# Optimization experiments

Measured on AMD Instinct MI355X. Metric: run time of the kernel, lower is better.

Reference implementation:

```python
import jax, jax.numpy as jnp
import numpy as np

N = 8192          # total genes
B = 16            # number of ragged batch groups (equal-size here: 512 each)
D = 768           # hidden_dim
NEG = -1.0e9      # mask fill value used by the original module


def setup_inputs() -> dict:
    key = jax.random.key(0)
    ks = jax.random.split(key, 10)
    s = 0.02
    inp = {
        "gene_embeddings": jax.random.normal(ks[0], (N, D), dtype=jnp.float32),
        # sorted group ids: 16 contiguous groups of 512 genes
        "batch": (jnp.arange(N) // (N // B)).astype(jnp.int64),
        "Wq": jax.random.normal(ks[1], (D, D), dtype=jnp.float32) * s,
        "bq": jnp.zeros((D,), dtype=jnp.float32),
        "Wk": jax.random.normal(ks[2], (D, D), dtype=jnp.float32) * s,
        "bk": jnp.zeros((D,), dtype=jnp.float32),
        "Wv": jax.random.normal(ks[3], (D, D), dtype=jnp.float32) * s,
        "bv": jnp.zeros((D,), dtype=jnp.float32),
        "Wo": jax.random.normal(ks[4], (D, D), dtype=jnp.float32) * s,
        "bo": jnp.zeros((D,), dtype=jnp.float32),
        "beta": jnp.ones((1,), dtype=jnp.float32) * 0.1,
    }
    return inp


def reference(gene_embeddings, batch, Wq, bq, Wk, bk, Wv, bv, Wo, bo, beta):
    # Single-head attention over full hidden_dim (num_heads unused in original).
    x = gene_embeddings
    q = x @ Wq.T + bq                      # [N, D]
    k = x @ Wk.T + bk
    v = x @ Wv.T + bv
    scale = 1.0 / jnp.sqrt(jnp.asarray(D, dtype=x.dtype))
    scores = (q @ k.T) * scale             # [N, N]
    # block-diagonal group mask + diagonal self-mask (same -1e9 fill as torch code)
    same_group = batch[:, None] == batch[None, :]
    eye = jnp.eye(N, dtype=bool)
    allow = same_group & (~eye)
    scores = jnp.where(allow, scores, NEG)
    weights = jax.nn.softmax(scores, axis=-1)   # dropout in eval mode -> identity
    dyn = weights @ v                       # [N, D]
    dyn = dyn @ Wo.T + bo
    return x + beta * dyn
```

## Files before the change

### kernel.cpp

```cpp
#include <hip/hip_runtime.h>
#include <hip/hip_bf16.h>
#include <cstdint>

using u16 = unsigned short;
using u32 = unsigned int;

typedef __bf16 bf16x8 __attribute__((ext_vector_type(8)));
typedef float  f32x4  __attribute__((ext_vector_type(4)));

__device__ __forceinline__ u32 f2b2(float a, float b) {
    __hip_bfloat162 h = __float22bfloat162_rn(float2{a, b});
    u32 u;
    __builtin_memcpy(&u, &h, 4);
    return u;
}
__device__ __forceinline__ float b2f(u16 b) {
    u32 u = (u32)b << 16;
    float f;
    __builtin_memcpy(&f, &u, 4);
    return f;
}

__device__ __forceinline__ void gload_lds16(const u16* g, u16* l) {
    __builtin_amdgcn_global_load_lds(
        (const __attribute__((address_space(1))) void*)g,
        (__attribute__((address_space(3))) void*)l,
        16, 0, 0);
}

__launch_bounds__(256)
__global__ void pack_kernel(const float* __restrict__ x,
                            const float* __restrict__ Wq,
                            const float* __restrict__ Wk,
                            const float* __restrict__ Wv,
                            const float* __restrict__ Wo,
                            const float* __restrict__ bq,
                            const float* __restrict__ bk,
                            const float* __restrict__ bv,
                            const float* __restrict__ bo,
                            u16* __restrict__ xb,
                            u16* __restrict__ Wqkvb,
                            u16* __restrict__ Wob,
                            u16* __restrict__ WvTb,
                            float* __restrict__ bqk,
                            float* __restrict__ bvoo)
{
    __shared__ u16 tl[64][72];
    const int b = blockIdx.x, tid = threadIdx.x;

    if (b < 3936) {
        int c = b * 256 + tid;
        long e = (long)c * 8;
        const float* src; u16* dst; long off;
        if (e < 6291456L)      { src = x;  dst = xb;             off = e; }
        else if (e < 6881280L) { src = Wq; dst = Wqkvb;          off = e - 6291456L; }
        else if (e < 7471104L) { src = Wk; dst = Wqkvb + 589824; off = e - 6881280L; }
        else                   { src = Wo; dst = Wob;            off = e - 7471104L; }
        float4 v0 = *(const float4*)(src + off);
        float4 v1 = *(const float4*)(src + off + 4);
        uint4 o;
        o.x = f2b2(v0.x, v0.y); o.y = f2b2(v0.z, v0.w);
        o.z = f2b2(v1.x, v1.y); o.w = f2b2(v1.z, v1.w);
        *(uint4*)(dst + off) = o;
        if (c < 768)       bqk[c] = bq[c];
        else if (c < 1536) bqk[c] = bk[c - 768];
    } else if (b < 4080) {
        int t = b - 3936;
        int tr = t / 12, tc = t % 12;
        int lr = tid >> 2, lcb = (tid & 3) * 16;
        const float* src = Wv + (long)(tr * 64 + lr) * 768 + tc * 64 + lcb;
#pragma unroll
        for (int q = 0; q < 4; q++) {
            float4 v = *(const float4*)(src + q * 4);
            u32 p0 = f2b2(v.x, v.y), p1 = f2b2(v.z, v.w);
            tl[lr][lcb + q * 4 + 0] = (u16)p0;
            tl[lr][lcb + q * 4 + 1] = (u16)(p0 >> 16);
            tl[lr][lcb + q * 4 + 2] = (u16)p1;
            tl[lr][lcb + q * 4 + 3] = (u16)(p1 >> 16);
        }
        __syncthreads();
        int li = tid >> 2, lkb = (tid & 3) * 16;
        u16 o[16];
#pragma unroll
        for (int j = 0; j < 16; j++) o[j] = tl[lkb + j][li];
        u16* dst = WvTb + (long)(tc * 64 + li) * 768 + tr * 64 + lkb;
#pragma unroll
        for (int j = 0; j < 16; j++) dst[j] = o[j];
    } else {
        int wave = tid >> 6, lane = tid & 63;
        int j = (b - 4080) * 4 + wave;
        float acc = 0.f;
#pragma unroll
        for (int i = 0; i < 12; i++) {
            int k = i * 64 + lane;
            acc += Wo[(long)j * 768 + k] * bv[k];
        }
#pragma unroll
        for (int d = 32; d; d >>= 1) acc += __shfl_xor(acc, d);
        if (lane == 0) bvoo[j] = acc + bo[j];
    }
}

template<int TM, int TN, int MODE>
__device__ __forceinline__ void gemm_body(
        const u16* __restrict__ A, int lda, long sAz,
        const u16* __restrict__ B, int ldb, long sBz,
        void* __restrict__ Cv, int ldc, long sCz,
        int K,
        const float* __restrict__ bias,
        float scale,
        u16* __restrict__ vTout)
{
    constexpr int FI = TM / 32;
    constexpr int FJ = TN / 32;
    constexpr int CA = TM / 64;
    constexpr int CB = TN / 64;

    __shared__ u16 As[2][TM * 32];
    __shared__ u16 Bs[2][TN * 32];

    const int tid  = threadIdx.x;
    const int g    = blockIdx.z;
    const u16* Ab = A + (long)g * sAz + (long)blockIdx.y * TM * lda;
    const u16* Bb = B + (long)g * sBz + (long)blockIdx.x * TN * ldb;

    const int wave = tid >> 6, lane = tid & 63;
    const int wm = (wave >> 1) * (TM / 2), wn = (wave & 1) * (TN / 2);
    const int ln15 = lane & 15, lq = lane >> 4;

    f32x4 acc[FI][FJ];
#pragma unroll
    for (int i = 0; i < FI; i++)
#pragma unroll
        for (int j = 0; j < FJ; j++)
            acc[i][j] = (f32x4){0.f, 0.f, 0.f, 0.f};

    const int srow = lane >> 2;
    const int sc   = ((lane & 3) ^ ((lane >> 4) & 3)) * 8;
    const u16* Ag[CA]; const u16* Bg[CB];
    int Al[CA], Bl[CB];
#pragma unroll
    for (int t = 0; t < CA; t++) {
        int c = wave * CA + t;
        Ag[t] = Ab + (long)(c * 16 + srow) * lda + sc;
        Al[t] = c * 512;
    }
#pragma unroll
    for (int t = 0; t < CB; t++) {
        int c = wave * CB + t;
        Bg[t] = Bb + (long)(c * 16 + srow) * ldb + sc;
        Bl[t] = c * 512;
    }

    const int foff = ln15 * 32 + ((lq ^ (ln15 >> 2)) * 8);
    const int nk = K >> 5;

#pragma unroll
    for (int t = 0; t < CA; t++) gload_lds16(Ag[t], &As[0][Al[t]]);
#pragma unroll
    for (int t = 0; t < CB; t++) gload_lds16(Bg[t], &Bs[0][Bl[t]]);

    for (int kt = 0; kt < nk; kt++) {
        const int cur = kt & 1;
        __syncthreads();
        if (kt + 1 < nk) {
            const int k0 = (kt + 1) * 32, nxt = cur ^ 1;
#pragma unroll
            for (int t = 0; t < CA; t++) gload_lds16(Ag[t] + k0, &As[nxt][Al[t]]);
#pragma unroll
            for (int t = 0; t < CB; t++) gload_lds16(Bg[t] + k0, &Bs[nxt][Bl[t]]);
        }

        bf16x8 af[FI], bfr[FJ];
#pragma unroll
        for (int i = 0; i < FI; i++)
            af[i] = *(const bf16x8*)&As[cur][(wm / 16 + i) * 512 + foff];
#pragma unroll
        for (int j = 0; j < FJ; j++)
            bfr[j] = *(const bf16x8*)&Bs[cur][(wn / 16 + j) * 512 + foff];
#pragma unroll
        for (int i = 0; i < FI; i++)
#pragma unroll
            for (int j = 0; j < FJ; j++)
                acc[i][j] = __builtin_amdgcn_mfma_f32_16x16x32_bf16(af[i], bfr[j], acc[i][j], 0, 0, 0);
    }

    const int baseRow = blockIdx.y * TM + wm;
    const int baseCol = blockIdx.x * TN + wn;

    if constexpr (MODE == 0) {
        if (baseCol < 1536) {
            u16* C = (u16*)Cv;
#pragma unroll
            for (int i = 0; i < FI; i++)
#pragma unroll
                for (int j = 0; j < FJ; j++) {
                    int col = baseCol + j * 16 + ln15;
                    float bb = bias[col];
                    u32 p01 = f2b2(acc[i][j][0] + bb, acc[i][j][1] + bb);
                    u32 p23 = f2b2(acc[i][j][2] + bb, acc[i][j][3] + bb);
                    long r0 = (long)(baseRow + i * 16 + lq * 4) * ldc + col;
                    C[r0]           = (u16)p01;
                    C[r0 + ldc]     = (u16)(p01 >> 16);
                    C[r0 + 2 * ldc] = (u16)p23;
                    C[r0 + 3 * ldc] = (u16)(p23 >> 16);
                }
        } else {
#pragma unroll
            for (int i = 0; i < FI; i++)
#pragma unroll
                for (int j = 0; j < FJ; j++) {
                    int col = baseCol + j * 16 + ln15;
                    uint2 o;
                    o.x = f2b2(acc[i][j][0], acc[i][j][1]);
                    o.y = f2b2(acc[i][j][2], acc[i][j][3]);
                    *(uint2*)(vTout + (long)(col - 1536) * 8192
                              + baseRow + i * 16 + lq * 4) = o;
                }
        }
    } else if constexpr (MODE == 5) {
        u16* C = (u16*)Cv + (long)g * sCz;
#pragma unroll
        for (int i = 0; i < FI; i++)
#pragma unroll
            for (int j = 0; j < FJ; j++) {
                int col = baseCol + j * 16 + ln15;
                float v[4];
#pragma unroll
                for (int r = 0; r < 4; r++) {
                    int row = baseRow + i * 16 + lq * 4 + r;
                    v[r] = acc[i][j][r] * scale;
                    if (row == col) v[r] = -1.0e9f;
                }
                u32 p01 = f2b2(v[0], v[1]);
                u32 p23 = f2b2(v[2], v[3]);
                long r0 = (long)(baseRow + i * 16 + lq * 4) * ldc + col;
                C[r0]           = (u16)p01;
                C[r0 + ldc]     = (u16)(p01 >> 16);
                C[r0 + 2 * ldc] = (u16)p23;
                C[r0 + 3 * ldc] = (u16)(p23 >> 16);
            }
    } else {
        u16* C = (u16*)Cv;
#pragma unroll
        for (int i = 0; i < FI; i++)
#pragma unroll
            for (int j = 0; j < FJ; j++) {
                int col = baseCol + j * 16 + ln15;
                u32 p01 = f2b2(acc[i][j][0], acc[i][j][1]);
                u32 p23 = f2b2(acc[i][j][2], acc[i][j][3]);
                long r0 = (long)(baseRow + i * 16 + lq * 4) * ldc + col;
                C[r0]           = (u16)p01;
                C[r0 + ldc]     = (u16)(p01 >> 16);
                C[r0 + 2 * ldc] = (u16)p23;
                C[r0 + 3 * ldc] = (u16)(p23 >> 16);
            }
    }
}

__launch_bounds__(256)
__global__ void k_wvo(const u16* A, const u16* B, void* C)
{
    gemm_body<64, 128, 3>(A, 768, 0, B, 768, 0, C, 768, 0, 768,
                          nullptr, 0.f, nullptr);
}
__launch_bounds__(256)
__global__ void k_qkv(const u16* A, const u16* B, void* C, const float* bias,
                      u16* vTout)
{
    gemm_body<128, 128, 0>(A, 768, 0, B, 768, 0, C, 1536, 0, 768,
                           bias, 0.f, vTout);
}
__launch_bounds__(256)
__global__ void k_scores(const u16* A, const u16* B, void* C, float scale)
{
    gemm_body<64, 128, 5>(A, 1536, 512L * 1536, B, 1536, 512L * 1536,
                          C, 512, 512L * 512, 768,
                          nullptr, scale, nullptr);
}

__launch_bounds__(256)
__global__ void k_pvwfused(const u16* __restrict__ S,
                           const u16* __restrict__ vwT,
                           const u16* __restrict__ xb,
                           float* __restrict__ out,
                           const float* __restrict__ bvoo,
                           const float* __restrict__ betaPtr)
{
    __shared__ u16 Pl[32 * 512];
    __shared__ u16 Vs[2][128 * 32];

    const int ct = blockIdx.x, rt = blockIdx.y, g = blockIdx.z;
    const int tid = threadIdx.x;
    const int wave = tid >> 6, lane = tid & 63;
    const int ln15 = lane & 15, lq = lane >> 4;

    const int srow = lane >> 2;
    const int sc   = ((lane & 3) ^ ((lane >> 4) & 3)) * 8;
    const u16* Bg[2]; int Bl[2];
#pragma unroll
    for (int t = 0; t < 2; t++) {
        int c = wave * 2 + t;
        Bg[t] = vwT + (long)(ct * 128 + c * 16 + srow) * 8192 + g * 512 + sc;
        Bl[t] = c * 512;
    }
    gload_lds16(Bg[0], &Vs[0][Bl[0]]);
    gload_lds16(Bg[1], &Vs[0][Bl[1]]);

    const int r   = tid >> 3;
    const int seg = tid & 7;
    const u16* Srow = S + (long)g * 262144 + (long)(rt * 32 + r) * 512 + seg * 64;
    float e[64];
    float m = -3.0e38f;
#pragma unroll
    for (int j = 0; j < 8; j++) {
        uint4 q = *(const uint4*)(Srow + j * 8);
        u32 w[4] = {q.x, q.y, q.z, q.w};
#pragma unroll
        for (int h = 0; h < 4; h++) {
            float lo = b2f((u16)w[h]);
            float hi = b2f((u16)(w[h] >> 16));
            e[j * 8 + h * 2]     = lo;
            e[j * 8 + h * 2 + 1] = hi;
            m = fmaxf(m, fmaxf(lo, hi));
        }
    }
    m = fmaxf(m, __shfl_xor(m, 1));
    m = fmaxf(m, __shfl_xor(m, 2));
    m = fmaxf(m, __shfl_xor(m, 4));
    float sum = 0.f;
#pragma unroll
    for (int j = 0; j < 64; j++) { e[j] = __expf(e[j] - m); sum += e[j]; }
    sum += __shfl_xor(sum, 1);
    sum += __shfl_xor(sum, 2);
    sum += __shfl_xor(sum, 4);
    const float inv = 1.0f / sum;
#pragma unroll
    for (int jj = 0; jj < 8; jj++) {
        uint4 o;
        o.x = f2b2(e[jj * 8 + 0] * inv, e[jj * 8 + 1] * inv);
        o.y = f2b2(e[jj * 8 + 2] * inv, e[jj * 8 + 3] * inv);
        o.z = f2b2(e[jj * 8 + 4] * inv, e[jj * 8 + 5] * inv);
        o.w = f2b2(e[jj * 8 + 6] * inv, e[jj * 8 + 7] * inv);
        int c = seg * 8 + jj;
        *(uint4*)&Pl[(r * 64 + (c ^ (r & 7))) * 8] = o;
    }

    const int wm = (wave >> 1) * 16;
    const int wn = (wave & 1) * 64;
    const int foff = ln15 * 32 + ((lq ^ (ln15 >> 2)) * 8);
    const int prow = wm + ln15;

    f32x4 acc[4];
#pragma unroll
    for (int j = 0; j < 4; j++) acc[j] = (f32x4){0.f, 0.f, 0.f, 0.f};

    for (int kt = 0; kt < 16; kt++) {
        const int cur = kt & 1;
        __syncthreads();
        if (kt + 1 < 16) {
            const int k0 = (kt + 1) * 32, nxt = cur ^ 1;
            gload_lds16(Bg[0] + k0, &Vs[nxt][Bl[0]]);
            gload_lds16(Bg[1] + k0, &Vs[nxt][Bl[1]]);
        }
        bf16x8 ap = *(const bf16x8*)&Pl[(prow * 64 + ((kt * 4 + lq) ^ (prow & 7))) * 8];
        bf16x8 bfr[4];
#pragma unroll
        for (int j = 0; j < 4; j++)
            bfr[j] = *(const bf16x8*)&Vs[cur][(wn / 16 + j) * 512 + foff];
#pragma unroll
        for (int j = 0; j < 4; j++)
            acc[j] = __builtin_amdgcn_mfma_f32_16x16x32_bf16(ap, bfr[j], acc[j], 0, 0, 0);
    }

    const float bet = betaPtr[0];
    const long rowBase = (long)(g * 512 + rt * 32 + wm + lq * 4);
    const u16* Xr = xb + rowBase * 768;
    float* O = out + rowBase * 768;
#pragma unroll
    for (int j = 0; j < 4; j++) {
        int col = ct * 128 + wn + j * 16 + ln15;
        float bb = bvoo[col];
#pragma unroll
        for (int rr = 0; rr < 4; rr++)
            O[rr * 768 + col] = b2f(Xr[rr * 768 + col])
                                + bet * (acc[j][rr] + bb);
    }
}

extern "C" void kernel_launch(void* const* d_in, const int* in_sizes, int n_in,
                              void* d_out, int out_size, void* d_ws, size_t ws_size,
                              hipStream_t stream)
{
    const float* x    = (const float*)d_in[0];
    const float* Wq   = (const float*)d_in[2];
    const float* bq   = (const float*)d_in[3];
    const float* Wk   = (const float*)d_in[4];
    const float* bk   = (const float*)d_in[5];
    const float* Wv   = (const float*)d_in[6];
    const float* bv   = (const float*)d_in[7];
    const float* Wo   = (const float*)d_in[8];
    const float* bo   = (const float*)d_in[9];
    const float* beta = (const float*)d_in[10];
    float* out = (float*)d_out;

    char* ws = (char*)d_ws;
    u16*   qk    = (u16*)(ws + 0);
    u16*   vwT   = (u16*)(ws + 25165824);
    u16*   xb    = (u16*)(ws + 37748736);
    u16*   S     = (u16*)(ws + 50331648);
    u16*   Wqkvb = (u16*)(ws + 58720256);
    u16*   Wob   = (u16*)(ws + 62259200);
    u16*   WvTb  = (u16*)(ws + 63438848);
    float* bqk   = (float*)(ws + 64618496);
    float* bvoo  = (float*)(ws + 64624640);

    const float scale = 0.03608439182435161f;

    pack_kernel<<<4272, 256, 0, stream>>>(x, Wq, Wk, Wv, Wo, bq, bk, bv, bo,
                                          xb, Wqkvb, Wob, WvTb, bqk, bvoo);

    k_wvo<<<dim3(6, 12, 1), 256, 0, stream>>>(Wob, WvTb,
                                              (void*)(Wqkvb + 1536L * 768));

    k_qkv<<<dim3(18, 64, 1), 256, 0, stream>>>(xb, Wqkvb, (void*)qk, bqk, vwT);

    k_scores<<<dim3(4, 8, 16), 256, 0, stream>>>(qk, qk + 768, (void*)S, scale);

    k_pvwfused<<<dim3(6, 16, 16), 256, 0, stream>>>(S, vwT, xb, out, bvoo, beta);
}
```

Baseline: 213.5 us.

## Fold Wk^T Wq into a single projection so scores use z·x instead of q·k

Rewrites the attention scores as (x·Wq^T Wk + bq·Wk)·x^T. Since bk only adds a per-row constant, it cancels in the softmax. A batched weight-weight GEMM now precomputes both Wk^T·Wq and Wo·Wv together, so the projection GEMM outputs only z and the V·Wo product (1536 columns instead of 2304). The score GEMM then reads the bf16 x directly as its key operand. This cuts one of three N×D×D projection GEMMs and shrinks intermediate traffic, at the cost of a larger combined weight GEMM and extra bf16 rounding of the fused weight product.

```diff
diff --git a/kernel.cpp b/kernel.cpp
--- a/kernel.cpp
+++ b/kernel.cpp
@@ -35,40 +35,39 @@
                             const float* __restrict__ Wv,
                             const float* __restrict__ Wo,
                             const float* __restrict__ bq,
-                            const float* __restrict__ bk,
                             const float* __restrict__ bv,
                             const float* __restrict__ bo,
                             u16* __restrict__ xb,
-                            u16* __restrict__ Wqkvb,
                             u16* __restrict__ Wob,
-                            u16* __restrict__ WvTb,
-                            float* __restrict__ bqk,
+                            u16* __restrict__ WqT,
+                            u16* __restrict__ WkT,
+                            u16* __restrict__ WvT,
+                            float* __restrict__ czk,
                             float* __restrict__ bvoo)
 {
     __shared__ u16 tl[64][72];
     const int b = blockIdx.x, tid = threadIdx.x;
 
-    if (b < 3936) {
+    if (b < 3360) {
         int c = b * 256 + tid;
         long e = (long)c * 8;
         const float* src; u16* dst; long off;
-        if (e < 6291456L)      { src = x;  dst = xb;             off = e; }
-        else if (e < 6881280L) { src = Wq; dst = Wqkvb;          off = e - 6291456L; }
-        else if (e < 7471104L) { src = Wk; dst = Wqkvb + 589824; off = e - 6881280L; }
-        else                   { src = Wo; dst = Wob;            off = e - 7471104L; }
+        if (e < 6291456L) { src = x;  dst = xb;  off = e; }
+        else              { src = Wo; dst = Wob; off = e - 6291456L; }
         float4 v0 = *(const float4*)(src + off);
         float4 v1 = *(const float4*)(src + off + 4);
         uint4 o;
         o.x = f2b2(v0.x, v0.y); o.y = f2b2(v0.z, v0.w);
         o.z = f2b2(v1.x, v1.y); o.w = f2b2(v1.z, v1.w);
         *(uint4*)(dst + off) = o;
-        if (c < 768)       bqk[c] = bq[c];
-        else if (c < 1536) bqk[c] = bk[c - 768];
-    } else if (b < 4080) {
-        int t = b - 3936;
-        int tr = t / 12, tc = t % 12;
+    } else if (b < 3792) {
+        int t = b - 3360;
+        int w = t / 144, tt = t % 144;
+        int tr = tt / 12, tc = tt % 12;
+        const float* src0 = (w == 0) ? Wq : (w == 1) ? Wk : Wv;
+        u16* dst0 = (w == 0) ? WqT : (w == 1) ? WkT : WvT;
         int lr = tid >> 2, lcb = (tid & 3) * 16;
-        const float* src = Wv + (long)(tr * 64 + lr) * 768 + tc * 64 + lcb;
+        const float* src = src0 + (long)(tr * 64 + lr) * 768 + tc * 64 + lcb;
 #pragma unroll
         for (int q = 0; q < 4; q++) {
             float4 v = *(const float4*)(src + q * 4);
@@ -83,12 +82,24 @@
         u16 o[16];
 #pragma unroll
         for (int j = 0; j < 16; j++) o[j] = tl[lkb + j][li];
-        u16* dst = WvTb + (long)(tc * 64 + li) * 768 + tr * 64 + lkb;
+        u16* dst = dst0 + (long)(tc * 64 + li) * 768 + tr * 64 + lkb;
 #pragma unroll
         for (int j = 0; j < 16; j++) dst[j] = o[j];
+    } else if (b < 3984) {
+        int wave = tid >> 6, lane = tid & 63;
+        int j = (b - 3792) * 4 + wave;
+        float acc = 0.f;
+#pragma unroll
+        for (int i = 0; i < 12; i++) {
+            int rr = i * 64 + lane;
+            acc += Wk[(long)rr * 768 + j] * bq[rr];
+        }
+#pragma unroll
+        for (int d = 32; d; d >>= 1) acc += __shfl_xor(acc, d);
+        if (lane == 0) czk[j] = acc;
     } else {
         int wave = tid >> 6, lane = tid & 63;
-        int j = (b - 4080) * 4 + wave;
+        int j = (b - 3984) * 4 + wave;
         float acc = 0.f;
 #pragma unroll
         for (int i = 0; i < 12; i++) {
@@ -189,7 +200,7 @@
     const int baseCol = blockIdx.x * TN + wn;
 
     if constexpr (MODE == 0) {
-        if (baseCol < 1536) {
+        if (baseCol < 768) {
             u16* C = (u16*)Cv;
 #pragma unroll
             for (int i = 0; i < FI; i++)
@@ -214,7 +225,7 @@
                     uint2 o;
                     o.x = f2b2(acc[i][j][0], acc[i][j][1]);
                     o.y = f2b2(acc[i][j][2], acc[i][j][3]);
-                    *(uint2*)(vTout + (long)(col - 1536) * 8192
+                    *(uint2*)(vTout + (long)(col - 768) * 8192
                               + baseRow + i * 16 + lq * 4) = o;
                 }
         }
@@ -241,7 +252,7 @@
                 C[r0 + 3 * ldc] = (u16)(p23 >> 16);
             }
     } else {
-        u16* C = (u16*)Cv;
+        u16* C = (u16*)Cv + (long)g * sCz;
 #pragma unroll
         for (int i = 0; i < FI; i++)
 #pragma unroll
@@ -259,33 +270,34 @@
 }
 
 __launch_bounds__(256)
-__global__ void k_wvo(const u16* A, const u16* B, void* C)
-{
-    gemm_body<64, 128, 3>(A, 768, 0, B, 768, 0, C, 768, 0, 768,
+__global__ void k_ww(const u16* WA, const u16* WB, void* WZplus)
+{
+    gemm_body<64, 128, 3>(WA, 768, 589824L, WB, 768, 589824L,
+                          WZplus, 768, -589824L, 768,
                           nullptr, 0.f, nullptr);
 }
 __launch_bounds__(256)
-__global__ void k_qkv(const u16* A, const u16* B, void* C, const float* bias,
-                      u16* vTout)
-{
-    gemm_body<128, 128, 0>(A, 768, 0, B, 768, 0, C, 1536, 0, 768,
+__global__ void k_zv(const u16* A, const u16* B, void* C, const float* bias,
+                     u16* vTout)
+{
+    gemm_body<128, 128, 0>(A, 768, 0, B, 768, 0, C, 768, 0, 768,
                            bias, 0.f, vTout);
 }
 __launch_bounds__(256)
 __global__ void k_scores(const u16* A, const u16* B, void* C, float scale)
 {
-    gemm_body<64, 128, 5>(A, 1536, 512L * 1536, B, 1536, 512L * 1536,
+    gemm_body<64, 128, 5>(A, 768, 512L * 768, B, 768, 512L * 768,
                           C, 512, 512L * 512, 768,
                           nullptr, scale, nullptr);
 }
 
 __launch_bounds__(256)
-__global__ void k_pvwfused(const u16* __restrict__ S,
-                           const u16* __restrict__ vwT,
-                           const u16* __restrict__ xb,
-                           float* __restrict__ out,
-                           const float* __restrict__ bvoo,
-                           const float* __restrict__ betaPtr)
+__global__ void k_pvw(const u16* __restrict__ S,
+                      const u16* __restrict__ vwT,
+                      const u16* __restrict__ xb,
+                      float* __restrict__ out,
+                      const float* __restrict__ bvoo,
+                      const float* __restrict__ betaPtr)
 {
     __shared__ u16 Pl[32 * 512];
     __shared__ u16 Vs[2][128 * 32];
@@ -403,29 +415,34 @@
     const float* bo   = (const float*)d_in[9];
     const float* beta = (const float*)d_in[10];
     float* out = (float*)d_out;
+    (void)bk;
 
     char* ws = (char*)d_ws;
-    u16*   qk    = (u16*)(ws + 0);
-    u16*   vwT   = (u16*)(ws + 25165824);
-    u16*   xb    = (u16*)(ws + 37748736);
-    u16*   S     = (u16*)(ws + 50331648);
-    u16*   Wqkvb = (u16*)(ws + 58720256);
-    u16*   Wob   = (u16*)(ws + 62259200);
-    u16*   WvTb  = (u16*)(ws + 63438848);
-    float* bqk   = (float*)(ws + 64618496);
-    float* bvoo  = (float*)(ws + 64624640);
+    u16*   zbuf = (u16*)(ws + 0);
+    u16*   vwT  = (u16*)(ws + 12582912);
+    u16*   xb   = (u16*)(ws + 25165824);
+    u16*   S    = (u16*)(ws + 37748736);
+    u16*   WA   = (u16*)(ws + 46137344);
+    u16*   WB   = (u16*)(ws + 48496640);
+    u16*   WZ   = (u16*)(ws + 50855936);
+    float* czk  = (float*)(ws + 53215232);
+    float* bvoo = (float*)(ws + 53218304);
+
+    u16* Wob = WA;
+    u16* WkT = WA + 589824;
+    u16* WvT = WB;
+    u16* WqT = WB + 589824;
 
     const float scale = 0.03608439182435161f;
 
-    pack_kernel<<<4272, 256, 0, stream>>>(x, Wq, Wk, Wv, Wo, bq, bk, bv, bo,
-                                          xb, Wqkvb, Wob, WvTb, bqk, bvoo);
-
-    k_wvo<<<dim3(6, 12, 1), 256, 0, stream>>>(Wob, WvTb,
-                                              (void*)(Wqkvb + 1536L * 768));
-
-    k_qkv<<<dim3(18, 64, 1), 256, 0, stream>>>(xb, Wqkvb, (void*)qk, bqk, vwT);
-
-    k_scores<<<dim3(4, 8, 16), 256, 0, stream>>>(qk, qk + 768, (void*)S, scale);
-
-    k_pvwfused<<<dim3(6, 16, 16), 256, 0, stream>>>(S, vwT, xb, out, bvoo, beta);
-}
+    pack_kernel<<<4176, 256, 0, stream>>>(x, Wq, Wk, Wv, Wo, bq, bv, bo,
+                                          xb, Wob, WqT, WkT, WvT, czk, bvoo);
+
+    k_ww<<<dim3(6, 12, 2), 256, 0, stream>>>(WA, WB, (void*)(WZ + 589824L));
+
+    k_zv<<<dim3(12, 64, 1), 256, 0, stream>>>(xb, WZ, (void*)zbuf, czk, vwT);
+
+    k_scores<<<dim3(4, 8, 16), 256, 0, stream>>>(zbuf, xb, (void*)S, scale);
+
+    k_pvw<<<dim3(6, 16, 16), 256, 0, stream>>>(S, vwT, xb, out, bvoo, beta);
+}
```

After: 207.0 us. -3.0%, faster.
